# Performance work log

Measured on AMD Instinct MI355X. Metric: run time of the kernel, lower is better.

The kernel has to match this reference:

```python
import jax, jax.numpy as jnp
import numpy as np

EPS_ATTN = 1e-5   # attention denominator eps (module eps)
EPS_LN = 1e-5     # nn.LayerNorm default eps


def _prime(x, proj):
    # Performer FAVOR+ hyperbolic positive features.
    # x: (B,H,L,dh), proj: (dh,m) -> (B,H,L,2m)
    dn = x.shape[-1] ** -0.25
    xn = dn * x
    d = jnp.einsum('bhld,dm->bhlm', xn, proj)
    diag = 0.5 * jnp.sum(xn * xn, axis=-1, keepdims=True)
    return jnp.concatenate([jnp.exp(d - diag), jnp.exp(-d - diag)], axis=-1)


def setup_inputs() -> dict:
    L, B, H, DH, DM, M = 2048, 4, 8, 64, 512, 256
    key = jax.random.key(0)
    k0, k1, k2 = jax.random.split(key, 3)
    h = jax.random.normal(k0, (L, B, DM), jnp.float32)
    w_qkv = jax.random.normal(k1, (H * 3 * DH, DM), jnp.float32) / np.sqrt(DM)
    w_o = jax.random.normal(k2, (DM, H * DH), jnp.float32) / np.sqrt(H * DH)
    ln_gamma = jnp.ones((DM,), jnp.float32)
    ln_beta = jnp.zeros((DM,), jnp.float32)
    # Gaussian orthogonal random matrix (blockwise QR), rows scaled by sqrt(dh)
    rng = np.random.default_rng(0)
    blocks = []
    for _ in range(M // DH):
        g = rng.standard_normal((DH, DH)).astype(np.float32)
        q, _ = np.linalg.qr(g)
        blocks.append(q.T)
    pm = np.concatenate(blocks, axis=0) * np.sqrt(DH)  # (M, DH)
    proj_matrix = jnp.asarray(pm.T.astype(np.float32))  # (DH, M)
    return {"h": h, "w_qkv": w_qkv, "w_o": w_o,
            "ln_gamma": ln_gamma, "ln_beta": ln_beta,
            "proj_matrix": proj_matrix}


def _forward(h, w_qkv, w_o, ln_gamma, ln_beta, proj_matrix):
    L, B, DM = h.shape
    DH, M = proj_matrix.shape
    H = w_qkv.shape[0] // (3 * DH)
    scale = DH ** -0.5

    qkv = (h @ w_qkv.T).reshape(L, B, H, 3 * DH)
    q, k, v = jnp.split(qkv, 3, axis=-1)
    q = jnp.transpose(q, (1, 2, 0, 3))  # (B,H,L,dh)
    k = jnp.transpose(k, (1, 2, 0, 3))
    v = jnp.transpose(v, (1, 2, 0, 3))

    qp = _prime(q, proj_matrix)  # (B,H,L,2M)
    kp = _prime(k, proj_matrix)
    kp = kp / jnp.sum(kp, axis=-1, keepdims=True)
    qp = qp / jnp.sum(qp, axis=-1, keepdims=True)

    den_acc = jnp.cumsum(kp, axis=2)
    denom = jnp.einsum('bhlm,bhlm->bhl', den_acc, qp)[..., None]  # (B,H,L,1)

    # fast_weight_sum: W_t = W_{t-1} + k_t v_t^T ; out_t = q_t @ W_t
    def step(W, xs):
        qt, kt, vt = xs  # (B,H,2M), (B,H,2M), (B,H,dh)
        W = W + kt[..., :, None] * vt[..., None, :]
        out = jnp.einsum('bhm,bhmd->bhd', qt, W)
        return W, out

    W0 = jnp.zeros((B, H, 2 * M, DH), h.dtype)
    xs = (jnp.transpose(qp, (2, 0, 1, 3)),
          jnp.transpose(kp, (2, 0, 1, 3)),
          jnp.transpose(v, (2, 0, 1, 3)))
    _, out = jax.lax.scan(step, W0, xs)  # (L,B,H,dh)
    out = jnp.transpose(out, (1, 2, 0, 3))  # (B,H,L,dh)

    out = scale * out / (denom + EPS_ATTN)
    out = jnp.transpose(out, (0, 2, 1, 3)).reshape(B, L, H * DH)  # (B,L,H*dh)
    out = jnp.swapaxes(out, 0, 1)  # (L,B,H*dh)

    attn_out = out @ w_o.T
    x = h + attn_out
    mu = jnp.mean(x, axis=-1, keepdims=True)
    var = jnp.mean((x - mu) ** 2, axis=-1, keepdims=True)
    return (x - mu) / jnp.sqrt(var + EPS_LN) * ln_gamma + ln_beta


def reference(h, w_qkv, w_o, ln_gamma, ln_beta, proj_matrix):
    return _forward(h, w_qkv, w_o, ln_gamma, ln_beta, proj_matrix)
```

## Files before the change

### kernel.cpp

```cpp
#include <hip/hip_runtime.h>
#include <hip/hip_fp16.h>
#include <math.h>

#define LSEQ 2048
#define NB 4
#define NH 8
#define DMID 512
#define CHK 128
#define SCALE 0.125f
#define DN 0.35355339059327373f
#define DN2 0.125f
#define LOG2E 1.4426950408889634f
#define EPS_ATTN 1e-5f
#define EPS_LN 1e-5f

typedef _Float16 f16x8 __attribute__((ext_vector_type(8)));
typedef _Float16 f16x4 __attribute__((ext_vector_type(4)));
typedef float f32x4 __attribute__((ext_vector_type(4)));

__device__ __forceinline__ float exp2a(float x) {
  float r;
  asm("v_exp_f32 %0, %1" : "=v"(r) : "v"(x));
  return r;
}

__device__ __forceinline__ void cvt16(const float* __restrict__ p,
                                      _Float16* __restrict__ dst) {
  float4 a = *(const float4*)p, b = *(const float4*)(p + 4);
  float4 c = *(const float4*)(p + 8), d = *(const float4*)(p + 12);
  f16x8 t0 = {(_Float16)a.x, (_Float16)a.y, (_Float16)a.z, (_Float16)a.w,
              (_Float16)b.x, (_Float16)b.y, (_Float16)b.z, (_Float16)b.w};
  f16x8 t1 = {(_Float16)c.x, (_Float16)c.y, (_Float16)c.z, (_Float16)c.w,
              (_Float16)d.x, (_Float16)d.y, (_Float16)d.z, (_Float16)d.w};
  *(f16x8*)dst = t0;
  *(f16x8*)(dst + 8) = t1;
}

__global__ void k_diag(float* out, int n, float val) {
  int i = blockIdx.x * 256 + threadIdx.x;
  if (i < n) out[i] = val;
}

__global__ __launch_bounds__(256) void k_ptr(const float* __restrict__ proj,
                                             __half* __restrict__ projT) {
  int e = blockIdx.x * 256 + threadIdx.x;
  int n = e >> 6, k = e & 63;
  projT[e] = __float2half_rn(proj[k * 256 + n] * (DN * LOG2E));
}

__global__ __launch_bounds__(256) void k_qkv(
    const float* __restrict__ A, const float* __restrict__ Wq,
    __half* __restrict__ q, __half* __restrict__ k, __half* __restrict__ v) {
  __shared__ __align__(16) char smem[34816];
  _Float16* Ah = (_Float16*)smem;
  _Float16* Bh = (_Float16*)(smem + 10240);
  _Float16* Oh = (_Float16*)smem;

  const int tid = threadIdx.x;
  const int row0 = blockIdx.x * 128;
  const int col0 = blockIdx.y * 128;
  const int lane = tid & 63, wv = tid >> 6;
  const int ln15 = lane & 15, quad = lane >> 4;
  const int m0 = wv * 32;
  const int srow = tid >> 1, sc = (tid & 1) * 16;

  f32x4 Cacc[2][8];
  const f32x4 z4 = {0.f, 0.f, 0.f, 0.f};
#pragma unroll
  for (int mi = 0; mi < 2; ++mi)
#pragma unroll
    for (int nt = 0; nt < 8; ++nt) Cacc[mi][nt] = z4;

  for (int kt = 0; kt < DMID; kt += 32) {
    cvt16(A + (size_t)(row0 + srow) * DMID + kt + sc, &Ah[srow * 40 + sc]);
    cvt16(Wq + (size_t)(col0 + srow) * DMID + kt + sc, &Bh[srow * 40 + sc]);
    __syncthreads();
    f16x8 a0 = *(const f16x8*)&Ah[(m0 + ln15) * 40 + quad * 8];
    f16x8 a1 = *(const f16x8*)&Ah[(m0 + 16 + ln15) * 40 + quad * 8];
#pragma unroll
    for (int nt = 0; nt < 8; ++nt) {
      f16x8 bf = *(const f16x8*)&Bh[(nt * 16 + ln15) * 40 + quad * 8];
      Cacc[0][nt] = __builtin_amdgcn_mfma_f32_16x16x32_f16(a0, bf, Cacc[0][nt], 0, 0, 0);
      Cacc[1][nt] = __builtin_amdgcn_mfma_f32_16x16x32_f16(a1, bf, Cacc[1][nt], 0, 0, 0);
    }
    __syncthreads();
  }
#pragma unroll
  for (int mi = 0; mi < 2; ++mi)
#pragma unroll
    for (int nt = 0; nt < 8; ++nt)
#pragma unroll
      for (int r = 0; r < 4; ++r)
        Oh[(m0 + mi * 16 + quad * 4 + r) * 136 + nt * 16 + ln15] =
            (_Float16)Cacc[mi][nt][r];
  __syncthreads();
  const int tr = tid >> 4, tc = tid & 15;
  const int col = col0 + tc * 8;
  const int hh = col / 192;
  const int rem = col - hh * 192;
  const int t = rem >> 6;
  const int d0 = rem & 63;
  __half* dstb = (t == 0) ? q : ((t == 1) ? k : v);
#pragma unroll
  for (int i = 0; i < 8; ++i) {
    int lrow = tr * 8 + i;
    int grow = row0 + lrow;
    int l = grow >> 2, bb = grow & 3;
    f16x8 val = *(const f16x8*)&Oh[lrow * 136 + tc * 8];
    *(f16x8*)((_Float16*)dstb + (((size_t)(bb * NH + hh) * LSEQ + l) << 6) + d0) = val;
  }
}

__global__ __launch_bounds__(512) void k_dgemm(
    const __half* __restrict__ qsrc, const __half* __restrict__ ksrc,
    const __half* __restrict__ projT, __half* __restrict__ dqd,
    __half* __restrict__ dkd, float* __restrict__ nq,
    float* __restrict__ nk) {
  __shared__ __align__(16) char smem[37888];
  _Float16* Bt = (_Float16*)smem;
  float* g_l  = (float*)(smem + 36864);
  float* ps_l = (float*)(smem + 37376);
  _Float16* Oh = (_Float16*)smem;

  const int tid = threadIdx.x;
  const __half* src = blockIdx.y ? ksrc : qsrc;
  __half* dst = blockIdx.y ? dkd : dqd;
  float* nrm = blockIdx.y ? nk : nq;
  const size_t r0 = (size_t)blockIdx.x * 128;

  const int lane = tid & 63, wv = tid >> 6;
  const int ln15 = lane & 15, quad = lane >> 4;
  const int m0 = wv * 16;

#pragma unroll
  for (int it = 0; it < 4; ++it) {
    int e = it * 512 + tid;
    int n = e >> 3, seg = e & 7;
    *(f16x8*)&Bt[n * 72 + seg * 8] =
        *(const f16x8*)((const _Float16*)projT + n * 64 + seg * 8);
  }

  f16x8 afrag[2];
  float ss = 0.f;
  {
    const _Float16* rp = (const _Float16*)src + (r0 + m0 + ln15) * 64;
#pragma unroll
    for (int ks = 0; ks < 2; ++ks) {
      f16x8 x8 = *(const f16x8*)(rp + ks * 32 + quad * 8);
      afrag[ks] = x8;
#pragma unroll
      for (int j = 0; j < 8; ++j) {
        float xv = (float)x8[j];
        ss = fmaf(xv, xv, ss);
      }
    }
    ss += __shfl_xor(ss, 16);
    ss += __shfl_xor(ss, 32);
  }
  if (quad == 0) g_l[m0 + ln15] = 0.5f * DN2 * LOG2E * ss;
  __syncthreads();

  f32x4 Cacc[16];
  const f32x4 z4 = {0.f, 0.f, 0.f, 0.f};
#pragma unroll
  for (int nt = 0; nt < 16; ++nt) Cacc[nt] = z4;

#pragma unroll
  for (int ks = 0; ks < 2; ++ks) {
    f16x8 a0 = afrag[ks];
#pragma unroll
    for (int nt = 0; nt < 16; ++nt) {
      f16x8 bf = *(const f16x8*)&Bt[(nt * 16 + ln15) * 72 + ks * 32 + quad * 8];
      Cacc[nt] = __builtin_amdgcn_mfma_f32_16x16x32_f16(a0, bf, Cacc[nt], 0, 0, 0);
    }
  }

  float gv[4], pp[4];
#pragma unroll
  for (int r = 0; r < 4; ++r) {
    gv[r] = g_l[m0 + quad * 4 + r];
    pp[r] = 0.f;
  }
#pragma unroll
  for (int nt = 0; nt < 16; ++nt)
#pragma unroll
    for (int r = 0; r < 4; ++r) {
      float d = Cacc[nt][r];
      pp[r] += exp2a(d - gv[r]) + exp2a(-d - gv[r]);
    }
#pragma unroll
  for (int r = 0; r < 4; ++r) {
    float p = pp[r];
    p += __shfl_xor(p, 1); p += __shfl_xor(p, 2);
    p += __shfl_xor(p, 4); p += __shfl_xor(p, 8);
    if (ln15 == 0) ps_l[m0 + quad * 4 + r] = p;
  }

#pragma unroll
  for (int hf = 0; hf < 2; ++hf) {
    __syncthreads();
#pragma unroll
    for (int nt2 = 0; nt2 < 8; ++nt2) {
      int nt = hf * 8 + nt2;
#pragma unroll
      for (int r = 0; r < 4; ++r)
        Oh[(m0 + quad * 4 + r) * 136 + nt2 * 16 + ln15] =
            (_Float16)Cacc[nt][r];
    }
    __syncthreads();
#pragma unroll
    for (int it = 0; it < 4; ++it) {
      int e = it * 512 + tid;
      int row = e >> 4, seg = e & 15;
      *(f16x8*)((_Float16*)dst + (r0 + row) * 256 + hf * 128 + seg * 8) =
          *(const f16x8*)&Oh[row * 136 + seg * 8];
    }
  }
  if (tid < 128) nrm[r0 + tid] = g_l[tid] + __log2f(ps_l[tid]);
}

__global__ __launch_bounds__(256) void k_kv(
    const __half* __restrict__ dk, const float* __restrict__ nk,
    const __half* __restrict__ v, __half* __restrict__ KVt,
    float* __restrict__ Ks) {
  __shared__ __align__(16) char smem[53248];
  _Float16* kpT = (_Float16*)smem;
  _Float16* Vt  = (_Float16*)(smem + 34816);
  float* ck = (float*)(smem + 52224);
  _Float16* Oh2 = (_Float16*)smem;

  const int tid = threadIdx.x;
  const int cidx = blockIdx.x;
  const int i0 = blockIdx.y * 128;
  const float fsign = (i0 < 256) ? 1.f : -1.f;
  const int m0col = (i0 < 256) ? i0 : i0 - 256;
  const size_t rowbase = (size_t)cidx * CHK;

  if (tid < 128) ck[tid] = nk[rowbase + tid];
  __syncthreads();

  {
    const int srow = tid >> 1;
    const int scol = (tid & 1) * 64;
    float c = ck[srow];
    const _Float16* src =
        (const _Float16*)dk + (rowbase + srow) * 256 + m0col + scol;
#pragma unroll
    for (int it = 0; it < 8; ++it) {
      f16x8 d8 = *(const f16x8*)(src + it * 8);
#pragma unroll
      for (int j = 0; j < 8; ++j)
        kpT[(scol + it * 8 + j) * 136 + srow] =
            (_Float16)exp2a(fmaf((float)d8[j], fsign, -c));
    }
  }
  {
    int s = tid & 127, dq0 = (tid >> 7) * 32;
    const _Float16* vsrc = (const _Float16*)v + (rowbase + s) * 64 + dq0;
#pragma unroll
    for (int b8 = 0; b8 < 4; ++b8) {
      f16x8 v8 = ((const f16x8*)vsrc)[b8];
#pragma unroll
      for (int j = 0; j < 8; ++j)
        Vt[(dq0 + b8 * 8 + j) * 136 + s] = v8[j];
    }
  }
  __syncthreads();

  const int lane = tid & 63, wv = tid >> 6;
  const int ln15 = lane & 15, quad = lane >> 4;
  const int m0 = wv * 32;

  f32x4 Cacc[2][4], Kacc[2];
  const f32x4 z4 = {0.f, 0.f, 0.f, 0.f};
#pragma unroll
  for (int mi = 0; mi < 2; ++mi) {
#pragma unroll
    for (int nt = 0; nt < 4; ++nt) Cacc[mi][nt] = z4;
    Kacc[mi] = z4;
  }
  f16x8 bone;
#pragma unroll
  for (int j = 0; j < 8; ++j)
    bone[j] = (ln15 == 0) ? (_Float16)1.0f : (_Float16)0.0f;

#pragma unroll
  for (int ks = 0; ks < 4; ++ks) {
    f16x8 a0 = *(const f16x8*)&kpT[(m0 + ln15) * 136 + ks * 32 + quad * 8];
    f16x8 a1 = *(const f16x8*)&kpT[(m0 + 16 + ln15) * 136 + ks * 32 + quad * 8];
#pragma unroll
    for (int nt = 0; nt < 4; ++nt) {
      f16x8 bV = *(const f16x8*)&Vt[(nt * 16 + ln15) * 136 + ks * 32 + quad * 8];
      Cacc[0][nt] = __builtin_amdgcn_mfma_f32_16x16x32_f16(a0, bV, Cacc[0][nt], 0, 0, 0);
      Cacc[1][nt] = __builtin_amdgcn_mfma_f32_16x16x32_f16(a1, bV, Cacc[1][nt], 0, 0, 0);
    }
    Kacc[0] = __builtin_amdgcn_mfma_f32_16x16x32_f16(a0, bone, Kacc[0], 0, 0, 0);
    Kacc[1] = __builtin_amdgcn_mfma_f32_16x16x32_f16(a1, bone, Kacc[1], 0, 0, 0);
  }

  if (ln15 == 0) {
#pragma unroll
    for (int mi = 0; mi < 2; ++mi)
#pragma unroll
      for (int r = 0; r < 4; ++r)
        Ks[(size_t)cidx * 512 + i0 + m0 + mi * 16 + quad * 4 + r] = Kacc[mi][r];
  }
  __syncthreads();
#pragma unroll
  for (int mi = 0; mi < 2; ++mi)
#pragma unroll
    for (int nt = 0; nt < 4; ++nt) {
      f16x4 pack = {(_Float16)Cacc[mi][nt][0], (_Float16)Cacc[mi][nt][1],
                    (_Float16)Cacc[mi][nt][2], (_Float16)Cacc[mi][nt][3]};
      *(f16x4*)&Oh2[(nt * 16 + ln15) * 136 + m0 + mi * 16 + quad * 4] = pack;
    }
  __syncthreads();
  {
    int d = tid >> 2, part = tid & 3;
    _Float16* dstp =
        (_Float16*)KVt + (size_t)cidx * 32768 + d * 512 + i0 + part * 32;
    const _Float16* srcp = &Oh2[d * 136 + part * 32];
#pragma unroll
    for (int j = 0; j < 4; ++j)
      *(f16x8*)(dstp + j * 8) = *(const f16x8*)(srcp + j * 8);
  }
}

__global__ __launch_bounds__(256) void k_scan(__half2* __restrict__ KV2,
                                              float* __restrict__ Ks) {
  const int bh = blockIdx.x;
  const int tid = threadIdx.x;
  if (blockIdx.y < 32) {
    uint2* p = (uint2*)(KV2 + (size_t)bh * 262144) + (blockIdx.y * 256 + tid);
    uint2 raw[16];
#pragma unroll
    for (int c = 0; c < 16; ++c) raw[c] = p[c * 8192];
    float ax0 = 0.f, ay0 = 0.f, ax1 = 0.f, ay1 = 0.f;
#pragma unroll
    for (int c = 0; c < 16; ++c) {
      __half2 h0 = *(__half2*)&raw[c].x;
      __half2 h1 = *(__half2*)&raw[c].y;
      float2 f0 = __half22float2(h0), f1 = __half22float2(h1);
      __half2 o0 = __floats2half2_rn(ax0, ay0);
      __half2 o1 = __floats2half2_rn(ax1, ay1);
      uint2 o;
      o.x = *(unsigned*)&o0;
      o.y = *(unsigned*)&o1;
      p[c * 8192] = o;
      ax0 += f0.x; ay0 += f0.y; ax1 += f1.x; ay1 += f1.y;
    }
  } else {
    int i = (blockIdx.y - 32) * 256 + tid;
    float* pk = Ks + (size_t)bh * 8192 + i;
    float vs[16];
#pragma unroll
    for (int c = 0; c < 16; ++c) vs[c] = pk[c * 512];
    float a = 0.f;
#pragma unroll
    for (int c = 0; c < 16; ++c) { pk[c * 512] = a; a += vs[c]; }
  }
}

__global__ __launch_bounds__(512) void k_attn(
    const __half* __restrict__ dq, const __half* __restrict__ dk,
    const float* __restrict__ nq, const float* __restrict__ nk,
    const __half* __restrict__ v, const __half* __restrict__ KVt,
    const float* __restrict__ Kpre, float* __restrict__ outb) {
  __shared__ __align__(16) char smem[53760];
  _Float16* qpT = (_Float16*)(smem);
  _Float16* kpT = (_Float16*)(smem + 18432);
  _Float16* WT  = (_Float16*)(smem + 36864);
  float*    KpT = (float*)(smem + 46080);
  float* cq_l   = (float*)(smem + 46336);
  float* ck_l   = (float*)(smem + 46848);
  _Float16* S_h = (_Float16*)(smem);
  _Float16* Vt  = (_Float16*)(smem + 34816);
  float* den1_l = (float*)(smem + 52224);
  float* den2_l = (float*)(smem + 52736);
  float* invd_l = (float*)(smem + 53248);

  const int tid = threadIdx.x;
  const int cidx = blockIdx.x;
  const int cc = cidx & 15, bh = cidx >> 4;
  const size_t rowb = (size_t)cidx * 128;
  const int lane = tid & 63;
  const int wv = tid >> 6;
  const int H = wv >> 2;
  const int m0 = (wv & 3) * 16;
  const int ln15 = lane & 15, quad = lane >> 4;

  if (tid < 128) cq_l[tid] = nq[rowb + tid];
  else if (tid < 256) ck_l[tid - 128] = nk[rowb + tid - 128];
  __syncthreads();

  const int c8 = tid & 7;
  const int r9 = tid >> 3;
  const int csrc = (c8 & 3) * 8;
  const float sgnf = (c8 < 4) ? 1.f : -1.f;

  const _Float16* qsrc = (const _Float16*)dq + (rowb + r9) * 256 + csrc;
  const _Float16* ksrc = (const _Float16*)dk + (rowb + r9) * 256 + csrc;
  const _Float16* wsrc = (const _Float16*)KVt + (size_t)cidx * 32768 +
                         r9 * 512 + ((c8 < 4) ? 0 : 256) + csrc;
  const float* kpsrc = Kpre + (size_t)cidx * 512 +
                       ((tid < 32) ? tid : (tid < 64 ? 224 + tid : 0));

  float cq[2], ck2[2];
#pragma unroll
  for (int p = 0; p < 2; ++p) {
    cq[p] = cq_l[r9 + p * 64];
    ck2[p] = ck_l[r9 + p * 64];
  }

  f16x8 rq[2], rk[2];
#pragma unroll
  for (int p = 0; p < 2; ++p) {
    rq[p] = *(const f16x8*)(qsrc + p * 16384);
    rk[p] = *(const f16x8*)(ksrc + p * 16384);
  }

  f32x4 Sacc[8], Oacc[4], Dacc;
  const f32x4 z4 = {0.f, 0.f, 0.f, 0.f};
#pragma unroll
  for (int nt = 0; nt < 8; ++nt) Sacc[nt] = z4;
#pragma unroll
  for (int nt = 0; nt < 4; ++nt) Oacc[nt] = z4;
  Dacc = z4;

  const int NSw = H ? 8 : 4;

  for (int it = 0; it < 8; ++it) {
    const int kb = it * 32;
    f16x8 w0 = *(const f16x8*)(wsrc + kb);
    float kp = kpsrc[kb];

#pragma unroll
    for (int p = 0; p < 2; ++p) {
      f16x8 d = rq[p], t;
#pragma unroll
      for (int j = 0; j < 8; ++j)
        t[j] = (_Float16)exp2a(fmaf((float)d[j], sgnf, -cq[p]));
      *(f16x8*)&qpT[(r9 + p * 64) * 72 + c8 * 8] = t;
    }
#pragma unroll
    for (int p = 0; p < 2; ++p) {
      f16x8 d = rk[p], t;
#pragma unroll
      for (int j = 0; j < 8; ++j)
        t[j] = (_Float16)exp2a(fmaf((float)d[j], sgnf, -ck2[p]));
      *(f16x8*)&kpT[(r9 + p * 64) * 72 + c8 * 8] = t;
    }

    if (it < 7) {
#pragma unroll
      for (int p = 0; p < 2; ++p) {
        rq[p] = *(const f16x8*)(qsrc + p * 16384 + kb + 32);
        rk[p] = *(const f16x8*)(ksrc + p * 16384 + kb + 32);
      }
    }
    *(f16x8*)&WT[r9 * 72 + c8 * 8] = w0;
    if (tid < 64) KpT[tid] = kp;

    asm volatile("s_waitcnt lgkmcnt(0)" ::: "memory");
    __builtin_amdgcn_s_barrier();
    asm volatile("" ::: "memory");

#pragma unroll
    for (int ks = 0; ks < 2; ++ks) {
      f16x8 a0 = *(const f16x8*)&qpT[(H * 64 + m0 + ln15) * 72 + ks * 32 + quad * 8];
#pragma unroll
      for (int nt = 0; nt < 4; ++nt) {
        f16x8 bf = *(const f16x8*)&kpT[(nt * 16 + ln15) * 72 + ks * 32 + quad * 8];
        Sacc[nt] = __builtin_amdgcn_mfma_f32_16x16x32_f16(a0, bf, Sacc[nt], 0, 0, 0);
      }
      if (H) {
#pragma unroll
        for (int nt = 4; nt < 8; ++nt) {
          f16x8 bf = *(const f16x8*)&kpT[(nt * 16 + ln15) * 72 + ks * 32 + quad * 8];
          Sacc[nt] = __builtin_amdgcn_mfma_f32_16x16x32_f16(a0, bf, Sacc[nt], 0, 0, 0);
        }
      }
#pragma unroll
      for (int nt = 0; nt < 4; ++nt) {
        f16x8 bw = *(const f16x8*)&WT[(nt * 16 + ln15) * 72 + ks * 32 + quad * 8];
        Oacc[nt] = __builtin_amdgcn_mfma_f32_16x16x32_f16(a0, bw, Oacc[nt], 0, 0, 0);
      }
      f16x8 bk;
#pragma unroll
      for (int j = 0; j < 8; ++j)
        bk[j] = (ln15 == 0) ? (_Float16)KpT[ks * 32 + quad * 8 + j]
                            : (_Float16)0.f;
      Dacc = __builtin_amdgcn_mfma_f32_16x16x32_f16(a0, bk, Dacc, 0, 0, 0);
    }

    asm volatile("" ::: "memory");
    __builtin_amdgcn_s_barrier();
    asm volatile("" ::: "memory");
  }

  if (ln15 == 0) {
#pragma unroll
    for (int r = 0; r < 4; ++r)
      den2_l[H * 64 + m0 + quad * 4 + r] = Dacc[r];
  }
  {
    _Float16* S_me = S_h + H * 8704;
    float dp[4] = {0.f, 0.f, 0.f, 0.f};
#pragma unroll
    for (int nt = 0; nt < 8; ++nt) {
      if (nt < NSw) {
        int s = nt * 16 + ln15;
#pragma unroll
        for (int r = 0; r < 4; ++r) {
          int tl = m0 + quad * 4 + r;
          float vsv = (s <= H * 64 + tl) ? Sacc[nt][r] : 0.f;
          dp[r] += vsv;
          S_me[tl * 136 + s] = (_Float16)vsv;
        }
      }
    }
#pragma unroll
    for (int r = 0; r < 4; ++r) {
      float p = dp[r];
      p += __shfl_xor(p, 1); p += __shfl_xor(p, 2);
      p += __shfl_xor(p, 4); p += __shfl_xor(p, 8);
      if (ln15 == 0) den1_l[H * 64 + m0 + quad * 4 + r] = p;
    }
  }
  {
    int s = tid & 127, d0v = (tid >> 7) * 16;
    const _Float16* vsrc = (const _Float16*)v + (rowb + s) * 64 + d0v;
    f16x8 v0 = ((const f16x8*)vsrc)[0];
    f16x8 v1 = ((const f16x8*)vsrc)[1];
#pragma unroll
    for (int j = 0; j < 8; ++j) {
      Vt[(d0v + j) * 136 + s] = v0[j];
      Vt[(d0v + 8 + j) * 136 + s] = v1[j];
    }
  }
  __syncthreads();
  if (tid < 128)
    invd_l[tid] = SCALE / (den1_l[tid] + den2_l[tid] + EPS_ATTN);
  __syncthreads();
  {
    _Float16* S_me = S_h + H * 8704;
#pragma unroll
    for (int ks = 0; ks < 4; ++ks) {
      if (ks < (H ? 4 : 2)) {
        f16x8 aS0 = *(const f16x8*)&S_me[(m0 + ln15) * 136 + ks * 32 + quad * 8];
#pragma unroll
        for (int nt = 0; nt < 4; ++nt) {
          f16x8 bV = *(const f16x8*)&Vt[(nt * 16 + ln15) * 136 + ks * 32 + quad * 8];
          Oacc[nt] = __builtin_amdgcn_mfma_f32_16x16x32_f16(aS0, bV, Oacc[nt], 0, 0, 0);
        }
      }
    }
  }
  const int b = bh >> 3, hh = bh & 7;
  float ivv[4];
#pragma unroll
  for (int r = 0; r < 4; ++r)
    ivv[r] = invd_l[H * 64 + m0 + quad * 4 + r];
#pragma unroll
  for (int nt = 0; nt < 4; ++nt) {
    int dcol = nt * 16 + ln15;
#pragma unroll
    for (int r = 0; r < 4; ++r) {
      int l = cc * 128 + H * 64 + m0 + quad * 4 + r;
      outb[((size_t)l * 4 + b) * 512 + hh * 64 + dcol] = Oacc[nt][r] * ivv[r];
    }
  }
}

__global__ __launch_bounds__(256) void k_oproj(
    const float* __restrict__ A, const float* __restrict__ Wo,
    const float* __restrict__ hres, float* __restrict__ xout) {
  __shared__ __align__(16) char smem[34816];
  _Float16* Ah = (_Float16*)smem;
  _Float16* Bh = (_Float16*)(smem + 10240);
  _Float16* Oh = (_Float16*)smem;

  const int tid = threadIdx.x;
  const int row0 = blockIdx.x * 128;
  const int col0 = blockIdx.y * 128;
  const int lane = tid & 63, wv = tid >> 6;
  const int ln15 = lane & 15, quad = lane >> 4;
  const int m0 = wv * 32;
  const int srow = tid >> 1, sc = (tid & 1) * 16;

  f32x4 Cacc[2][8];
  const f32x4 z4 = {0.f, 0.f, 0.f, 0.f};
#pragma unroll
  for (int mi = 0; mi < 2; ++mi)
#pragma unroll
    for (int nt = 0; nt < 8; ++nt) Cacc[mi][nt] = z4;

  for (int kt = 0; kt < DMID; kt += 32) {
    cvt16(A + (size_t)(row0 + srow) * DMID + kt + sc, &Ah[srow * 40 + sc]);
    cvt16(Wo + (size_t)(col0 + srow) * DMID + kt + sc, &Bh[srow * 40 + sc]);
    __syncthreads();
    f16x8 a0 = *(const f16x8*)&Ah[(m0 + ln15) * 40 + quad * 8];
    f16x8 a1 = *(const f16x8*)&Ah[(m0 + 16 + ln15) * 40 + quad * 8];
#pragma unroll
    for (int nt = 0; nt < 8; ++nt) {
      f16x8 bf = *(const f16x8*)&Bh[(nt * 16 + ln15) * 40 + quad * 8];
      Cacc[0][nt] = __builtin_amdgcn_mfma_f32_16x16x32_f16(a0, bf, Cacc[0][nt], 0, 0, 0);
      Cacc[1][nt] = __builtin_amdgcn_mfma_f32_16x16x32_f16(a1, bf, Cacc[1][nt], 0, 0, 0);
    }
    __syncthreads();
  }
#pragma unroll
  for (int mi = 0; mi < 2; ++mi)
#pragma unroll
    for (int nt = 0; nt < 8; ++nt)
#pragma unroll
      for (int r = 0; r < 4; ++r)
        Oh[(m0 + mi * 16 + quad * 4 + r) * 136 + nt * 16 + ln15] =
            (_Float16)Cacc[mi][nt][r];
  __syncthreads();
  const int tr = tid >> 4, tc = tid & 15;
#pragma unroll
  for (int i = 0; i < 8; ++i) {
    int lrow = tr * 8 + i;
    int grow = row0 + lrow;
    size_t base = (size_t)grow * 512 + col0 + tc * 8;
    f16x8 o = *(const f16x8*)&Oh[lrow * 136 + tc * 8];
    float4 h0 = *(const float4*)(hres + base);
    float4 h1 = *(const float4*)(hres + base + 4);
    *(float4*)(xout + base) =
        make_float4((float)o[0] + h0.x, (float)o[1] + h0.y,
                    (float)o[2] + h0.z, (float)o[3] + h0.w);
    *(float4*)(xout + base + 4) =
        make_float4((float)o[4] + h1.x, (float)o[5] + h1.y,
                    (float)o[6] + h1.z, (float)o[7] + h1.w);
  }
}

__global__ __launch_bounds__(256) void k_ln(float* __restrict__ x,
                                            const float* __restrict__ g,
                                            const float* __restrict__ bta) {
  __shared__ float ws_[4], wq_[4];
  const int row = blockIdx.x;
  const int tid = threadIdx.x;
  float2 vv = *(const float2*)(x + (size_t)row * 512 + tid * 2);
  float s = vv.x + vv.y;
  float sq = vv.x * vv.x + vv.y * vv.y;
#pragma unroll
  for (int off = 1; off < 64; off <<= 1) {
    s += __shfl_xor(s, off, 64);
    sq += __shfl_xor(sq, off, 64);
  }
  if ((tid & 63) == 0) { ws_[tid >> 6] = s; wq_[tid >> 6] = sq; }
  __syncthreads();
  s = ws_[0] + ws_[1] + ws_[2] + ws_[3];
  sq = wq_[0] + wq_[1] + wq_[2] + wq_[3];
  float mu = s * (1.f / 512.f);
  float var = sq * (1.f / 512.f) - mu * mu;
  float rstd = rsqrtf(var + EPS_LN);
  int c = tid * 2;
  float2 o;
  o.x = (vv.x - mu) * rstd * g[c] + bta[c];
  o.y = (vv.y - mu) * rstd * g[c + 1] + bta[c + 1];
  *(float2*)(x + (size_t)row * 512 + c) = o;
}

extern "C" void kernel_launch(void* const* d_in, const int* in_sizes, int n_in,
                              void* d_out, int out_size, void* d_ws,
                              size_t ws_size, hipStream_t stream) {
  const float* h    = (const float*)d_in[0];
  const float* wqkv = (const float*)d_in[1];
  const float* wo   = (const float*)d_in[2];
  const float* g    = (const float*)d_in[3];
  const float* bta  = (const float*)d_in[4];
  const float* proj = (const float*)d_in[5];
  float* out = (float*)d_out;
  char* wsb = (char*)d_ws;

  __half* q   = (__half*)(wsb + 0);
  __half* kb  = (__half*)(wsb + 8388608);
  __half* vb  = (__half*)(wsb + 16777216);
  __half* dq  = (__half*)(wsb + 25165824);
  __half* dk  = (__half*)(wsb + 58720256);
  float*  nq  = (float*)(wsb + 92274688);
  float*  nk  = (float*)(wsb + 92798976);
  __half* KVt = (__half*)(wsb + 93323264);
  float*  Ks  = (float*)(wsb + 126877696);
  __half* pT  = (__half*)(wsb + 127926272);
  float* outb = (float*)(wsb + 0);

  if (ws_size < 127959040ull) {
    float val = 1000.0f + (float)(ws_size >> 20);
    k_diag<<<(out_size + 255) / 256, 256, 0, stream>>>(out, out_size, val);
    return;
  }

  k_ptr  <<<dim3(64), 256, 0, stream>>>(proj, pT);
  k_qkv  <<<dim3(64, 12), 256, 0, stream>>>(h, wqkv, q, kb, vb);
  k_dgemm<<<dim3(512, 2), 512, 0, stream>>>(q, kb, pT, dq, dk, nq, nk);
  k_kv   <<<dim3(512, 4), 256, 0, stream>>>(dk, nk, vb, KVt, Ks);
  k_scan <<<dim3(32, 34), 256, 0, stream>>>((__half2*)KVt, Ks);
  k_attn <<<dim3(512), 512, 0, stream>>>(dq, dk, nq, nk, vb, KVt, Ks, outb);
  k_oproj<<<dim3(64, 4), 256, 0, stream>>>(outb, wo, h, out);
  k_ln   <<<dim3(8192), 256, 0, stream>>>(out, g, bta);
}
```

Before: 243.7 us.

## Enlarge QKV GEMM row tile and merge KV feature blocks per chunk

The QKV projection now runs 512-thread blocks covering 256 rows, so each weight tile converted to LDS is reused across twice as many rows, and the output is staged through LDS in two halves. The chunked KV kernel now uses one 512-thread block per chunk that loads V once and walks all four feature slices (both signs, both halves), where before four blocks each reloaded V and re-read the same key rows. This cuts redundant global loads and launches. In exchange there are fewer blocks in flight and more barriers per block, which may reduce latency hiding.

Measured after the change: 239.2 us. No clear change (-1.9%).

```diff
diff --git a/kernel.cpp b/kernel.cpp
--- a/kernel.cpp
+++ b/kernel.cpp
@@ -48,21 +48,20 @@
   projT[e] = __float2half_rn(proj[k * 256 + n] * (DN * LOG2E));
 }
 
-__global__ __launch_bounds__(256) void k_qkv(
+__global__ __launch_bounds__(512) void k_qkv(
     const float* __restrict__ A, const float* __restrict__ Wq,
     __half* __restrict__ q, __half* __restrict__ k, __half* __restrict__ v) {
   __shared__ __align__(16) char smem[34816];
   _Float16* Ah = (_Float16*)smem;
-  _Float16* Bh = (_Float16*)(smem + 10240);
+  _Float16* Bh = (_Float16*)(smem + 20480);
   _Float16* Oh = (_Float16*)smem;
 
   const int tid = threadIdx.x;
-  const int row0 = blockIdx.x * 128;
+  const int row0 = blockIdx.x * 256;
   const int col0 = blockIdx.y * 128;
   const int lane = tid & 63, wv = tid >> 6;
   const int ln15 = lane & 15, quad = lane >> 4;
   const int m0 = wv * 32;
-  const int srow = tid >> 1, sc = (tid & 1) * 16;
 
   f32x4 Cacc[2][8];
   const f32x4 z4 = {0.f, 0.f, 0.f, 0.f};
@@ -71,9 +70,12 @@
 #pragma unroll
     for (int nt = 0; nt < 8; ++nt) Cacc[mi][nt] = z4;
 
+  const int sarow = tid >> 1, sac = (tid & 1) * 16;
   for (int kt = 0; kt < DMID; kt += 32) {
-    cvt16(A + (size_t)(row0 + srow) * DMID + kt + sc, &Ah[srow * 40 + sc]);
-    cvt16(Wq + (size_t)(col0 + srow) * DMID + kt + sc, &Bh[srow * 40 + sc]);
+    cvt16(A + (size_t)(row0 + sarow) * DMID + kt + sac, &Ah[sarow * 40 + sac]);
+    if (tid < 256)
+      cvt16(Wq + (size_t)(col0 + sarow) * DMID + kt + sac,
+            &Bh[sarow * 40 + sac]);
     __syncthreads();
     f16x8 a0 = *(const f16x8*)&Ah[(m0 + ln15) * 40 + quad * 8];
     f16x8 a1 = *(const f16x8*)&Ah[(m0 + 16 + ln15) * 40 + quad * 8];
@@ -85,15 +87,7 @@
     }
     __syncthreads();
   }
-#pragma unroll
-  for (int mi = 0; mi < 2; ++mi)
-#pragma unroll
-    for (int nt = 0; nt < 8; ++nt)
-#pragma unroll
-      for (int r = 0; r < 4; ++r)
-        Oh[(m0 + mi * 16 + quad * 4 + r) * 136 + nt * 16 + ln15] =
-            (_Float16)Cacc[mi][nt][r];
-  __syncthreads();
+
   const int tr = tid >> 4, tc = tid & 15;
   const int col = col0 + tc * 8;
   const int hh = col / 192;
@@ -101,13 +95,30 @@
   const int t = rem >> 6;
   const int d0 = rem & 63;
   __half* dstb = (t == 0) ? q : ((t == 1) ? k : v);
-#pragma unroll
-  for (int i = 0; i < 8; ++i) {
-    int lrow = tr * 8 + i;
-    int grow = row0 + lrow;
-    int l = grow >> 2, bb = grow & 3;
-    f16x8 val = *(const f16x8*)&Oh[lrow * 136 + tc * 8];
-    *(f16x8*)((_Float16*)dstb + (((size_t)(bb * NH + hh) * LSEQ + l) << 6) + d0) = val;
+
+#pragma unroll
+  for (int hf = 0; hf < 2; ++hf) {
+    if ((wv >> 2) == hf) {
+      int lm = (wv & 3) * 32;
+#pragma unroll
+      for (int mi = 0; mi < 2; ++mi)
+#pragma unroll
+        for (int nt = 0; nt < 8; ++nt)
+#pragma unroll
+          for (int r = 0; r < 4; ++r)
+            Oh[(lm + mi * 16 + quad * 4 + r) * 136 + nt * 16 + ln15] =
+                (_Float16)Cacc[mi][nt][r];
+    }
+    __syncthreads();
+#pragma unroll
+    for (int i = 0; i < 4; ++i) {
+      int lrow = tr * 4 + i;
+      int grow = row0 + hf * 128 + lrow;
+      int l = grow >> 2, bb = grow & 3;
+      f16x8 val = *(const f16x8*)&Oh[lrow * 136 + tc * 8];
+      *(f16x8*)((_Float16*)dstb + (((size_t)(bb * NH + hh) * LSEQ + l) << 6) + d0) = val;
+    }
+    __syncthreads();
   }
 }
 
@@ -219,11 +230,11 @@
   if (tid < 128) nrm[r0 + tid] = g_l[tid] + __log2f(ps_l[tid]);
 }
 
-__global__ __launch_bounds__(256) void k_kv(
+__global__ __launch_bounds__(512) void k_kv(
     const __half* __restrict__ dk, const float* __restrict__ nk,
     const __half* __restrict__ v, __half* __restrict__ KVt,
     float* __restrict__ Ks) {
-  __shared__ __align__(16) char smem[53248];
+  __shared__ __align__(16) char smem[52736];
   _Float16* kpT = (_Float16*)smem;
   _Float16* Vt  = (_Float16*)(smem + 34816);
   float* ck = (float*)(smem + 52224);
@@ -231,98 +242,96 @@
 
   const int tid = threadIdx.x;
   const int cidx = blockIdx.x;
-  const int i0 = blockIdx.y * 128;
-  const float fsign = (i0 < 256) ? 1.f : -1.f;
-  const int m0col = (i0 < 256) ? i0 : i0 - 256;
   const size_t rowbase = (size_t)cidx * CHK;
-
-  if (tid < 128) ck[tid] = nk[rowbase + tid];
-  __syncthreads();
-
-  {
-    const int srow = tid >> 1;
-    const int scol = (tid & 1) * 64;
-    float c = ck[srow];
-    const _Float16* src =
-        (const _Float16*)dk + (rowbase + srow) * 256 + m0col + scol;
-#pragma unroll
-    for (int it = 0; it < 8; ++it) {
-      f16x8 d8 = *(const f16x8*)(src + it * 8);
-#pragma unroll
-      for (int j = 0; j < 8; ++j)
-        kpT[(scol + it * 8 + j) * 136 + srow] =
-            (_Float16)exp2a(fmaf((float)d8[j], fsign, -c));
-    }
-  }
-  {
-    int s = tid & 127, dq0 = (tid >> 7) * 32;
-    const _Float16* vsrc = (const _Float16*)v + (rowbase + s) * 64 + dq0;
-#pragma unroll
-    for (int b8 = 0; b8 < 4; ++b8) {
-      f16x8 v8 = ((const f16x8*)vsrc)[b8];
-#pragma unroll
-      for (int j = 0; j < 8; ++j)
-        Vt[(dq0 + b8 * 8 + j) * 136 + s] = v8[j];
-    }
-  }
-  __syncthreads();
-
   const int lane = tid & 63, wv = tid >> 6;
   const int ln15 = lane & 15, quad = lane >> 4;
-  const int m0 = wv * 32;
-
-  f32x4 Cacc[2][4], Kacc[2];
-  const f32x4 z4 = {0.f, 0.f, 0.f, 0.f};
-#pragma unroll
-  for (int mi = 0; mi < 2; ++mi) {
-#pragma unroll
-    for (int nt = 0; nt < 4; ++nt) Cacc[mi][nt] = z4;
-    Kacc[mi] = z4;
-  }
+
+  if (tid < 128) ck[tid] = nk[rowbase + tid];
+  {
+    int s = tid & 127, dq0 = (tid >> 7) * 16;
+    const _Float16* vsrc = (const _Float16*)v + (rowbase + s) * 64 + dq0;
+    f16x8 v0 = ((const f16x8*)vsrc)[0];
+    f16x8 v1 = ((const f16x8*)vsrc)[1];
+#pragma unroll
+    for (int j = 0; j < 8; ++j) {
+      Vt[(dq0 + j) * 136 + s] = v0[j];
+      Vt[(dq0 + 8 + j) * 136 + s] = v1[j];
+    }
+  }
+
+  const int srow = tid >> 2;
+  const int scol = (tid & 3) * 32;
+
   f16x8 bone;
 #pragma unroll
   for (int j = 0; j < 8; ++j)
     bone[j] = (ln15 == 0) ? (_Float16)1.0f : (_Float16)0.0f;
 
-#pragma unroll
-  for (int ks = 0; ks < 4; ++ks) {
-    f16x8 a0 = *(const f16x8*)&kpT[(m0 + ln15) * 136 + ks * 32 + quad * 8];
-    f16x8 a1 = *(const f16x8*)&kpT[(m0 + 16 + ln15) * 136 + ks * 32 + quad * 8];
-#pragma unroll
-    for (int nt = 0; nt < 4; ++nt) {
-      f16x8 bV = *(const f16x8*)&Vt[(nt * 16 + ln15) * 136 + ks * 32 + quad * 8];
-      Cacc[0][nt] = __builtin_amdgcn_mfma_f32_16x16x32_f16(a0, bV, Cacc[0][nt], 0, 0, 0);
-      Cacc[1][nt] = __builtin_amdgcn_mfma_f32_16x16x32_f16(a1, bV, Cacc[1][nt], 0, 0, 0);
-    }
-    Kacc[0] = __builtin_amdgcn_mfma_f32_16x16x32_f16(a0, bone, Kacc[0], 0, 0, 0);
-    Kacc[1] = __builtin_amdgcn_mfma_f32_16x16x32_f16(a1, bone, Kacc[1], 0, 0, 0);
-  }
-
-  if (ln15 == 0) {
-#pragma unroll
-    for (int mi = 0; mi < 2; ++mi)
-#pragma unroll
-      for (int r = 0; r < 4; ++r)
-        Ks[(size_t)cidx * 512 + i0 + m0 + mi * 16 + quad * 4 + r] = Kacc[mi][r];
-  }
-  __syncthreads();
-#pragma unroll
-  for (int mi = 0; mi < 2; ++mi)
-#pragma unroll
-    for (int nt = 0; nt < 4; ++nt) {
-      f16x4 pack = {(_Float16)Cacc[mi][nt][0], (_Float16)Cacc[mi][nt][1],
-                    (_Float16)Cacc[mi][nt][2], (_Float16)Cacc[mi][nt][3]};
-      *(f16x4*)&Oh2[(nt * 16 + ln15) * 136 + m0 + mi * 16 + quad * 4] = pack;
-    }
-  __syncthreads();
-  {
-    int d = tid >> 2, part = tid & 3;
-    _Float16* dstp =
-        (_Float16*)KVt + (size_t)cidx * 32768 + d * 512 + i0 + part * 32;
-    const _Float16* srcp = &Oh2[d * 136 + part * 32];
-#pragma unroll
-    for (int j = 0; j < 4; ++j)
-      *(f16x8*)(dstp + j * 8) = *(const f16x8*)(srcp + j * 8);
+  bool first = true;
+#pragma unroll
+  for (int cp = 0; cp < 2; ++cp) {
+    f16x8 rk[4];
+    const _Float16* dsrc =
+        (const _Float16*)dk + (rowbase + srow) * 256 + cp * 128 + scol;
+#pragma unroll
+    for (int it = 0; it < 4; ++it) rk[it] = *(const f16x8*)(dsrc + it * 8);
+    float c = ck[srow];
+    if (first) { __syncthreads(); c = ck[srow]; }
+
+#pragma unroll
+    for (int sg = 0; sg < 2; ++sg) {
+      const int i0 = sg * 256 + cp * 128;
+      const float fsign = sg ? -1.f : 1.f;
+      if (!first) __syncthreads();
+      first = false;
+#pragma unroll
+      for (int it = 0; it < 4; ++it) {
+        f16x8 d8 = rk[it];
+#pragma unroll
+        for (int j = 0; j < 8; ++j)
+          kpT[(scol + it * 8 + j) * 136 + srow] =
+              (_Float16)exp2a(fmaf((float)d8[j], fsign, -c));
+      }
+      __syncthreads();
+
+      f32x4 Cacc[4], Kacc;
+      const f32x4 z4 = {0.f, 0.f, 0.f, 0.f};
+#pragma unroll
+      for (int nt = 0; nt < 4; ++nt) Cacc[nt] = z4;
+      Kacc = z4;
+#pragma unroll
+      for (int ks = 0; ks < 4; ++ks) {
+        f16x8 a0 = *(const f16x8*)&kpT[(wv * 16 + ln15) * 136 + ks * 32 + quad * 8];
+#pragma unroll
+        for (int nt = 0; nt < 4; ++nt) {
+          f16x8 bV = *(const f16x8*)&Vt[(nt * 16 + ln15) * 136 + ks * 32 + quad * 8];
+          Cacc[nt] = __builtin_amdgcn_mfma_f32_16x16x32_f16(a0, bV, Cacc[nt], 0, 0, 0);
+        }
+        Kacc = __builtin_amdgcn_mfma_f32_16x16x32_f16(a0, bone, Kacc, 0, 0, 0);
+      }
+      if (ln15 == 0) {
+#pragma unroll
+        for (int r = 0; r < 4; ++r)
+          Ks[(size_t)cidx * 512 + i0 + wv * 16 + quad * 4 + r] = Kacc[r];
+      }
+      __syncthreads();
+
+#pragma unroll
+      for (int nt = 0; nt < 4; ++nt) {
+        f16x4 pack = {(_Float16)Cacc[nt][0], (_Float16)Cacc[nt][1],
+                      (_Float16)Cacc[nt][2], (_Float16)Cacc[nt][3]};
+        *(f16x4*)&Oh2[(nt * 16 + ln15) * 136 + wv * 16 + quad * 4] = pack;
+      }
+      __syncthreads();
+      {
+        int d = tid >> 3, part = tid & 7;
+        _Float16* dstp =
+            (_Float16*)KVt + (size_t)cidx * 32768 + d * 512 + i0 + part * 16;
+        const _Float16* srcp = &Oh2[d * 136 + part * 16];
+        *(f16x8*)(dstp) = *(const f16x8*)(srcp);
+        *(f16x8*)(dstp + 8) = *(const f16x8*)(srcp + 8);
+      }
+    }
   }
 }
 
@@ -695,9 +704,9 @@
   }
 
   k_ptr  <<<dim3(64), 256, 0, stream>>>(proj, pT);
-  k_qkv  <<<dim3(64, 12), 256, 0, stream>>>(h, wqkv, q, kb, vb);
+  k_qkv  <<<dim3(32, 12), 512, 0, stream>>>(h, wqkv, q, kb, vb);
   k_dgemm<<<dim3(512, 2), 512, 0, stream>>>(q, kb, pT, dq, dk, nq, nk);
-  k_kv   <<<dim3(512, 4), 256, 0, stream>>>(dk, nk, vb, KVt, Ks);
+  k_kv   <<<dim3(512), 512, 0, stream>>>(dk, nk, vb, KVt, Ks);
   k_scan <<<dim3(32, 34), 256, 0, stream>>>((__half2*)KVt, Ks);
   k_attn <<<dim3(512), 512, 0, stream>>>(dq, dk, nq, nk, vb, KVt, Ks, outb);
   k_oproj<<<dim3(64, 4), 256, 0, stream>>>(outb, wo, h, out);
```
